# Kernel optimization log

Hardware: AMD Instinct MI355X
Metric: run time of the kernel (lower is better)

## Reference

```python
import jax, jax.numpy as jnp
import numpy as np
from jax import lax

TEMP = 20.0    # args.temp
ATT_WT = 0.5   # args.att_wt
EPS = 1e-12


def l2norm(x, axis):
    # torch F.normalize: x / max(||x||_2, eps)
    n = jnp.sqrt(jnp.sum(x * x, axis=axis, keepdims=True))
    return x / jnp.maximum(n, EPS)


def conv4d(x, w):
    """4D conv, padding=1, stride=1.
    x: [B,Cin,H1,W1,H2,W2], w: [Cout,Cin,3,3,3,3] -> [B,Cout,H1,W1,H2,W2].
    Decomposed as 9 fixed (di,dj) shifts over (H1,W1), each a 2D conv over (H2,W2).
    """
    B, Cin, H1, W1, H2, W2 = x.shape
    Cout = w.shape[0]
    xp = jnp.pad(x, ((0, 0), (0, 0), (1, 1), (1, 1), (0, 0), (0, 0)))
    out = jnp.zeros((B * H1 * W1, Cout, H2, W2), x.dtype)
    for di in range(3):
        for dj in range(3):
            xs = xp[:, :, di:di + H1, dj:dj + W1]                      # [B,Cin,H1,W1,H2,W2]
            xr = xs.transpose(0, 2, 3, 1, 4, 5).reshape(B * H1 * W1, Cin, H2, W2)
            out = out + lax.conv_general_dilated(
                xr, w[:, :, di, dj], (1, 1), 'SAME',
                dimension_numbers=('NCHW', 'OIHW', 'NCHW'))
    return out.reshape(B, H1, W1, Cout, H2, W2).transpose(0, 3, 1, 2, 4, 5)


def nc_stack(x, ws):
    for w in ws:
        x = jax.nn.relu(conv4d(x, w))
    return x


def neigh_consensus(corr, ws):
    # symmetric mode: conv(C) + perm(conv(perm(C)))
    ct = corr.transpose(0, 1, 4, 5, 2, 3)
    return nc_stack(corr, ws) + nc_stack(ct, ws).transpose(0, 1, 4, 5, 2, 3)


def setup_inputs() -> dict:
    key = jax.random.key(0)
    ks = jax.random.split(key, 7)
    L, B, C, h, w = 9, 2, 1024, 20, 20
    ch = 256
    return {
        'fq_feats': jax.random.normal(ks[0], (L, B, C, h, w), jnp.float32),
        'fs_feats': jax.random.normal(ks[1], (L, B, C, h, w), jnp.float32),
        'f_q': jax.random.normal(ks[2], (B, ch, h, w), jnp.float32),
        'f_s': jax.random.normal(ks[3], (B, ch, h, w), jnp.float32),
        'w1': jax.random.normal(ks[4], (10, 9, 3, 3, 3, 3), jnp.float32) * 0.1,
        'w2': jax.random.normal(ks[5], (10, 10, 3, 3, 3, 3), jnp.float32) * 0.1,
        'w3': jax.random.normal(ks[6], (1, 10, 3, 3, 3, 3), jnp.float32) * 0.1,
    }


def reference(fq_feats, fs_feats, f_q, f_s, w1, w2, w3):
    L, B, C, h, w = fq_feats.shape
    ch = f_q.shape[1]
    hw = h * w
    # per-level channel-wise L2 normalization -> cosine correlation volume
    fqn = l2norm(fq_feats, axis=2)
    fsn = l2norm(fs_feats, axis=2)
    # corr4d[b,l,i,j,k,m] = <fq[:, i,j], fs[:, k,m]>  -> [B, L, h, w, h, w]
    corr4d = jnp.einsum('lbcij,lbckm->blijkm', fqn, fsn)
    # neighbourhood-consensus matching net -> [B,1,h,w,h,w]
    c4 = neigh_consensus(corr4d, (w1, w2, w3))
    attn = jax.nn.softmax(c4.reshape(B, hw, hw) * TEMP, axis=-1)  # over support positions
    v = f_s.reshape(B, ch, hw)
    att_fq = jnp.einsum('bqs,bcs->bcq', attn, v).reshape(B, ch, h, w)
    fq = l2norm(f_q, axis=1) + l2norm(att_fq, axis=1) * ATT_WT
    return (fq, att_fq)
```

## Files before the change

kernel.cpp:

```cpp
#include <hip/hip_runtime.h>
#include <math.h>
#include <stddef.h>

#define L9   9
#define NB   2
#define CF   1024
#define HW   400
#define CH   256
#define TEMPF 20.0f
#define EPSF  1e-12f

typedef _Float16 half8 __attribute__((ext_vector_type(8)));
typedef float f32x4 __attribute__((ext_vector_type(4)));
typedef unsigned short ushort_t;

#define HALO_ZERO(NT)                                                          \
    for (int h = threadIdx.x; h < 84 * 20; h += (NT)) {                        \
        int rs = h / 20, c = h - rs * 20;                                      \
        int row = rs < 22 ? rs                                                 \
                : rs < 44 ? 440 + rs                                           \
                : rs < 64 ? (rs - 43) * 22                                     \
                          : (rs - 63) * 22 + 21;                               \
        ((uint*)Ah)[row * 20 + c] = 0;                                         \
    }

__global__ __launch_bounds__(256) void prep_all(const float* __restrict__ w1,
                                                const float* __restrict__ w2,
                                                const float* __restrict__ w3,
                                                const float* __restrict__ f_s,
                                                ushort_t* __restrict__ wb0,
                                                ushort_t* __restrict__ fsh,
                                                float* __restrict__ ssbuf) {
    int gid = blockIdx.x * 256 + threadIdx.x;
    if (gid < NB * CH * 416) {
        int s = gid % 416, bc = gid / 416;
        float v = (s < HW) ? f_s[(size_t)bc * HW + s] : 0.f;
        union { _Float16 h; ushort_t u; } cv; cv.h = (_Float16)v;
        fsh[gid] = cv.u;
    }
    if (gid < 14400) ssbuf[gid] = 0.f;
    if (gid < 6 * 18432) {
        int job = gid / 18432, idx = gid - job * 18432;
        int k = idx & 31, n = (idx >> 5) & 15, dd = (idx >> 9) % 9, ch = idx / 4608;
        int dk = dd / 3, dm = dd % 3;
        float v = 0.f;
        if (job < 4) {
            if (idx < 13824) {
                int CIN = (job < 2) ? 9 : 10;
                const float* wt = (job < 2) ? w1 : w2;
                bool swap = job & 1;
                int slot = ch * 32 + k;
                if (n < 10 && slot < CIN * 9) {
                    int ci = slot / 9, pl = slot - ci * 9;
                    int di = pl / 3, dj = pl % 3;
                    int widx = swap ? ((((n * CIN + ci) * 3 + dk) * 3 + dm) * 3 + di) * 3 + dj
                                    : ((((n * CIN + ci) * 3 + di) * 3 + dj) * 3 + dk) * 3 + dm;
                    v = wt[widx];
                }
                union { _Float16 h; ushort_t u; } cv; cv.h = (_Float16)v;
                wb0[job * 13824 + idx] = cv.u;
            }
        } else {
            bool swap = (job == 5);
            int slot = ch * 32 + k;
            if (slot < 120) {
                int ci = slot / 12, r = slot - ci * 12;
                int di = r >> 2, dj4 = r & 3;
                int e = dj4 - n;
                if (n < 2 && e >= 0 && e <= 2) {
                    int widx = swap ? (((ci * 3 + dk) * 3 + dm) * 3 + di) * 3 + e
                                    : (((ci * 3 + di) * 3 + e) * 3 + dk) * 3 + dm;
                    v = w3[widx];
                }
            }
            union { _Float16 h; ushort_t u; } cv; cv.h = (_Float16)v;
            wb0[55296 + (job - 4) * 18432 + idx] = cv.u;
        }
    }
}

__global__ __launch_bounds__(256) void transpose_f16(const float* __restrict__ fq,
                                                     const float* __restrict__ fs,
                                                     ushort_t* __restrict__ At,
                                                     ushort_t* __restrict__ Bt,
                                                     float* __restrict__ ssbuf,
                                                     int lb_base) {
    __shared__ float tile[64][65];
    __shared__ float red4[4][64];
    int z = blockIdx.z;
    int tsel = z / 9, li = z - tsel * 9;
    int lb = lb_base + li;
    const float* src = (tsel ? fs : fq) + (size_t)lb * CF * HW;
    ushort_t* dst = (tsel ? Bt : At) + (size_t)li * HW * CF;
    int c0 = blockIdx.x * 64, ij0 = blockIdx.y * 64;
    int tid = threadIdx.x;
    int cl = tid >> 6;
    int col = tid & 63;
    float ssp = 0.f;
    #pragma unroll
    for (int rr = 0; rr < 16; ++rr) {
        int c_local = rr * 4 + cl;
        int ij = ij0 + col;
        float v = (ij < HW) ? src[(size_t)(c0 + c_local) * HW + ij] : 0.f;
        tile[c_local][col] = v;
        ssp = fmaf(v, v, ssp);
    }
    red4[cl][col] = ssp;
    __syncthreads();
    if (cl == 0) {
        int ij = ij0 + col;
        if (ij < HW) {
            float s4 = red4[0][col] + red4[1][col] + red4[2][col] + red4[3][col];
            atomicAdd(&ssbuf[(size_t)(tsel * 18 + lb) * HW + ij], s4);
        }
    }
    int cp = (tid & 31) * 2;
    int rowsel = tid >> 5;
    #pragma unroll
    for (int rr = 0; rr < 8; ++rr) {
        int ij_local = rr * 8 + rowsel;
        int ij = ij0 + ij_local;
        if (ij < HW) {
            union { _Float16 h; ushort_t u; } h0, h1;
            h0.h = (_Float16)tile[cp][ij_local];
            h1.h = (_Float16)tile[cp + 1][ij_local];
            ushort2 o; o.x = h0.u; o.y = h1.u;
            *(ushort2*)(dst + (size_t)ij * CF + c0 + cp) = o;
        }
    }
}

__global__ __launch_bounds__(256) void corr_gemm_mfma(const ushort_t* __restrict__ At,
                                                      const ushort_t* __restrict__ Bt,
                                                      const float* __restrict__ ssbuf,
                                                      ushort_t* __restrict__ corr,
                                                      int lb_base) {
    __shared__ ushort_t As[32][72];
    __shared__ ushort_t Bs[64][72];
    int li = blockIdx.z, lb = lb_base + li;
    int l = lb >> 1, b = lb & 1;
    int i0 = blockIdx.y * 32, j0 = blockIdx.x * 64;
    int tid = threadIdx.x, lane = tid & 63, w = tid >> 6;
    int mw = (w >> 1) * 16, nw = (w & 1) * 32;
    f32x4 acc[2] = {};
    const ushort_t* Abase = At + (size_t)li * HW * CF;
    const ushort_t* Bbase = Bt + (size_t)li * HW * CF;

    for (int kt = 0; kt < 16; ++kt) {
        int c0 = kt * 64;
        __syncthreads();
        {
            int row = tid >> 3, c8 = tid & 7;
            uint4 va = make_uint4(0, 0, 0, 0);
            if (i0 + row < HW) va = *(const uint4*)(Abase + (size_t)(i0 + row) * CF + c0 + c8 * 8);
            *(uint4*)&As[row][c8 * 8] = va;
        }
        #pragma unroll
        for (int p = 0; p < 2; ++p) {
            int idx = tid + p * 256;
            int row = idx >> 3, c8 = idx & 7;
            uint4 vb = make_uint4(0, 0, 0, 0);
            if (j0 + row < HW) vb = *(const uint4*)(Bbase + (size_t)(j0 + row) * CF + c0 + c8 * 8);
            *(uint4*)&Bs[row][c8 * 8] = vb;
        }
        __syncthreads();
        #pragma unroll
        for (int ks = 0; ks < 2; ++ks) {
            int k0 = ks * 32 + (lane >> 4) * 8;
            half8 a0 = *(const half8*)&As[mw + (lane & 15)][k0];
            half8 b0 = *(const half8*)&Bs[nw + (lane & 15)][k0];
            half8 b1 = *(const half8*)&Bs[nw + 16 + (lane & 15)][k0];
            acc[0] = __builtin_amdgcn_mfma_f32_16x16x32_f16(a0, b0, acc[0], 0, 0, 0);
            acc[1] = __builtin_amdgcn_mfma_f32_16x16x32_f16(a0, b1, acc[1], 0, 0, 0);
        }
    }
    int obase = (b * 9 + l) * HW;
    #pragma unroll
    for (int ni = 0; ni < 2; ++ni) {
        int km = j0 + nw + ni * 16 + (lane & 15);
        if (km >= HW) continue;
        float ib = 1.0f / fmaxf(sqrtf(ssbuf[(size_t)(18 + lb) * HW + km]), EPSF);
        #pragma unroll
        for (int r = 0; r < 4; ++r) {
            int ij = i0 + mw + (lane >> 4) * 4 + r;
            if (ij < HW) {
                float ia = 1.0f / fmaxf(sqrtf(ssbuf[(size_t)lb * HW + ij]), EPSF);
                union { _Float16 h; ushort_t u; } cv;
                cv.h = (_Float16)(acc[ni][r] * ia * ib);
                corr[(size_t)(obase + ij) * HW + km] = cv.u;
            }
        }
    }
}

template <int CIN, int COUT, bool DUAL, bool OUTF16>
__global__ __launch_bounds__(256) void conv4d_v8h(const ushort_t* __restrict__ inA,
                                                  const ushort_t* __restrict__ inB,
                                                  const ushort_t* __restrict__ wbA,
                                                  const ushort_t* __restrict__ wbB,
                                                  void* __restrict__ outA,
                                                  void* __restrict__ outB) {
    constexpr int S = CIN * 9;
    constexpr int NCH = (S + 31) / 32;
    __shared__ __align__(16) ushort_t Ah[484 * 40];
    const int b = blockIdx.y, ij = blockIdx.x;
    const int z = blockIdx.z;
    const ushort_t* in = (DUAL || z == 0) ? inA : inB;
    const ushort_t* wbS = (DUAL || z == 0) ? wbA : wbB;
    void* outS = (DUAL || z == 0) ? outA : outB;
    const int i = ij / 20, j = ij - (ij / 20) * 20;
    const int tid = threadIdx.x, wv = tid >> 6, lane = tid & 63;
    const int m16 = lane & 15, q4 = lane >> 4;

    HALO_ZERO(256)

    int baseh[7];
    #pragma unroll
    for (int s = 0; s < 7; ++s) {
        int t = wv + 4 * s;
        if (t < 25) {
            int km = t * 16 + m16;
            int kk = km / 20, mm = km - kk * 20;
            baseh[s] = (kk * 22 + mm) * 40 + q4 * 8;
        } else baseh[s] = 0;
    }
    f32x4 accA[7] = {};
    f32x4 accB[7] = {};

    const bool stager = tid < 200;
    const int km1 = 2 * tid;
    const int r1 = stager ? ((km1 / 20 + 1) * 22 + (km1 % 20) + 1) : 0;
    int hofs[9]; bool vld[9];
    #pragma unroll
    for (int pl = 0; pl < 9; ++pl) {
        int ii = i + pl / 3 - 1, jj = j + pl % 3 - 1;
        vld[pl] = (unsigned)ii < 20u && (unsigned)jj < 20u;
        hofs[pl] = (ii * 20 + jj) * HW + km1;
    }
    const ushort_t* in_b = in + (size_t)b * CIN * HW * HW;
    const int wbase = m16 * 32 + q4 * 8;

    uint pf[32];
    #pragma unroll
    for (int u = 0; u < 32; ++u) {
        int slot = u;
        if (slot < S) {
            int ci = slot / 9, pl = slot - ci * 9;
            pf[u] = (stager && vld[pl]) ? *(const uint*)(in_b + ci * (HW * HW) + hofs[pl]) : 0u;
        } else pf[u] = 0u;
    }
    __syncthreads();

    #pragma unroll
    for (int ch = 0; ch < NCH; ++ch) {
        if (stager) {
            #pragma unroll
            for (int g4 = 0; g4 < 8; ++g4) {
                uint lo0 = (pf[4 * g4] & 0xFFFFu) | (pf[4 * g4 + 1] << 16);
                uint lo1 = (pf[4 * g4 + 2] & 0xFFFFu) | (pf[4 * g4 + 3] << 16);
                uint hi0 = (pf[4 * g4] >> 16) | (pf[4 * g4 + 1] & 0xFFFF0000u);
                uint hi1 = (pf[4 * g4 + 2] >> 16) | (pf[4 * g4 + 3] & 0xFFFF0000u);
                uint2 wlo; wlo.x = lo0; wlo.y = lo1;
                uint2 whi; whi.x = hi0; whi.y = hi1;
                *(uint2*)&Ah[(size_t)r1 * 40 + 4 * g4] = wlo;
                *(uint2*)&Ah[(size_t)(r1 + 1) * 40 + 4 * g4] = whi;
            }
        }
        __syncthreads();
        if (ch + 1 < NCH) {
            #pragma unroll
            for (int u = 0; u < 32; ++u) {
                int slot = (ch + 1) * 32 + u;
                if (slot < S) {
                    int ci = slot / 9, pl = slot - ci * 9;
                    pf[u] = (stager && vld[pl]) ? *(const uint*)(in_b + ci * (HW * HW) + hofs[pl]) : 0u;
                } else pf[u] = 0u;
            }
        }
        #pragma unroll
        for (int dd = 0; dd < 9; ++dd) {
            half8 bfA = *(const half8*)(wbS + (ch * 9 + dd) * 512 + wbase);
            half8 bfB;
            if (DUAL) bfB = *(const half8*)(wbB + (ch * 9 + dd) * 512 + wbase);
            const int doff = ((dd / 3) * 22 + (dd % 3)) * 40;
            #pragma unroll
            for (int s = 0; s < 7; ++s) {
                if (wv + 4 * s < 25) {
                    half8 af = *(const half8*)(Ah + baseh[s] + doff);
                    accA[s] = __builtin_amdgcn_mfma_f32_16x16x32_f16(af, bfA, accA[s], 0, 0, 0);
                    if (DUAL) accB[s] = __builtin_amdgcn_mfma_f32_16x16x32_f16(af, bfB, accB[s], 0, 0, 0);
                }
            }
        }
        if (ch + 1 < NCH) __syncthreads();
    }

    const int co = m16;
    if (co < COUT) {
        #pragma unroll
        for (int s = 0; s < 7; ++s) {
            int t = wv + 4 * s;
            if (t < 25) {
                int km0 = t * 16 + q4 * 4;
                size_t o = ((size_t)(b * COUT + co) * HW + ij) * HW + km0;
                if (OUTF16) {
                    union { ushort_t us[4]; uint2 u2; } pk;
                    #pragma unroll
                    for (int r = 0; r < 4; ++r) {
                        union { _Float16 h; ushort_t u16; } cv;
                        cv.h = (_Float16)fmaxf(accA[s][r], 0.f);
                        pk.us[r] = cv.u16;
                    }
                    *(uint2*)((ushort_t*)outS + o) = pk.u2;
                    if (DUAL) {
                        #pragma unroll
                        for (int r = 0; r < 4; ++r) {
                            union { _Float16 h; ushort_t u16; } cv;
                            cv.h = (_Float16)fmaxf(accB[s][r], 0.f);
                            pk.us[r] = cv.u16;
                        }
                        *(uint2*)((ushort_t*)outB + o) = pk.u2;
                    }
                } else {
                    f32x4 ov;
                    #pragma unroll
                    for (int r = 0; r < 4; ++r) ov[r] = fmaxf(accA[s][r], 0.f);
                    *(f32x4*)((float*)outS + o) = ov;
                }
            }
        }
    }
}

template <int CIN, int COUT, bool DUAL, bool OUTF16>
__global__ __launch_bounds__(512, 2) void conv4d_v14h(const ushort_t* __restrict__ inA,
                                                      const ushort_t* __restrict__ inB,
                                                      const ushort_t* __restrict__ wbA,
                                                      const ushort_t* __restrict__ wbB,
                                                      void* __restrict__ outA,
                                                      void* __restrict__ outB) {
    constexpr int S = CIN * 9;
    constexpr int NCH = (S + 31) / 32;
    __shared__ __align__(16) ushort_t Ah[484 * 40];
    const int b = blockIdx.y, ij = blockIdx.x;
    const int z = blockIdx.z;
    const ushort_t* in = (DUAL || z == 0) ? inA : inB;
    const ushort_t* wbS = (DUAL || z == 0) ? wbA : wbB;
    void* outS = (DUAL || z == 0) ? outA : outB;
    const int i = ij / 20, j = ij - (ij / 20) * 20;
    const int tid = threadIdx.x, wv = tid >> 6, lane = tid & 63;
    const int m16 = lane & 15, q4 = lane >> 4;
    const int wt = 7 - wv;

    HALO_ZERO(512)

    int baseh[4];
    #pragma unroll
    for (int s = 0; s < 4; ++s) {
        int t = wt + 8 * s;
        if (t < 25) {
            int km = t * 16 + m16;
            int kk = km / 20, mm = km - kk * 20;
            baseh[s] = (kk * 22 + mm) * 40 + q4 * 8;
        } else baseh[s] = 0;
    }
    f32x4 accA[4] = {};
    f32x4 accB[4] = {};

    const bool stager = tid < 200;
    const int km1 = 2 * tid;
    const int r1 = stager ? ((km1 / 20 + 1) * 22 + (km1 % 20) + 1) : 0;
    int hofs[9]; bool vld[9];
    #pragma unroll
    for (int pl = 0; pl < 9; ++pl) {
        int ii = i + pl / 3 - 1, jj = j + pl % 3 - 1;
        vld[pl] = (unsigned)ii < 20u && (unsigned)jj < 20u;
        hofs[pl] = (ii * 20 + jj) * HW + km1;
    }
    const ushort_t* in_b = in + (size_t)b * CIN * HW * HW;
    const int wbase = m16 * 32 + q4 * 8;

    uint pf[32];
    #pragma unroll
    for (int u = 0; u < 32; ++u) {
        int slot = u;
        if (slot < S) {
            int ci = slot / 9, pl = slot - ci * 9;
            pf[u] = (stager && vld[pl]) ? *(const uint*)(in_b + ci * (HW * HW) + hofs[pl]) : 0u;
        } else pf[u] = 0u;
    }
    __syncthreads();

    #pragma unroll
    for (int ch = 0; ch < NCH; ++ch) {
        if (stager) {
            #pragma unroll
            for (int g4 = 0; g4 < 8; ++g4) {
                uint lo0 = (pf[4 * g4] & 0xFFFFu) | (pf[4 * g4 + 1] << 16);
                uint lo1 = (pf[4 * g4 + 2] & 0xFFFFu) | (pf[4 * g4 + 3] << 16);
                uint hi0 = (pf[4 * g4] >> 16) | (pf[4 * g4 + 1] & 0xFFFF0000u);
                uint hi1 = (pf[4 * g4 + 2] >> 16) | (pf[4 * g4 + 3] & 0xFFFF0000u);
                uint2 wlo; wlo.x = lo0; wlo.y = lo1;
                uint2 whi; whi.x = hi0; whi.y = hi1;
                *(uint2*)&Ah[(size_t)r1 * 40 + 4 * g4] = wlo;
                *(uint2*)&Ah[(size_t)(r1 + 1) * 40 + 4 * g4] = whi;
            }
        }
        __syncthreads();
        if (ch + 1 < NCH) {
            #pragma unroll
            for (int u = 0; u < 32; ++u) {
                int slot = (ch + 1) * 32 + u;
                if (slot < S) {
                    int ci = slot / 9, pl = slot - ci * 9;
                    pf[u] = (stager && vld[pl]) ? *(const uint*)(in_b + ci * (HW * HW) + hofs[pl]) : 0u;
                } else pf[u] = 0u;
            }
        }
        #pragma unroll
        for (int dd = 0; dd < 9; ++dd) {
            half8 bfA = *(const half8*)(wbS + (ch * 9 + dd) * 512 + wbase);
            half8 bfB;
            if (DUAL) bfB = *(const half8*)(wbB + (ch * 9 + dd) * 512 + wbase);
            const int doff = ((dd / 3) * 22 + (dd % 3)) * 40;
            #pragma unroll
            for (int s = 0; s < 4; ++s) {
                if (wt + 8 * s < 25) {
                    half8 af = *(const half8*)(Ah + baseh[s] + doff);
                    accA[s] = __builtin_amdgcn_mfma_f32_16x16x32_f16(af, bfA, accA[s], 0, 0, 0);
                    if (DUAL) accB[s] = __builtin_amdgcn_mfma_f32_16x16x32_f16(af, bfB, accB[s], 0, 0, 0);
                }
            }
        }
        if (ch + 1 < NCH) __syncthreads();
    }

    const int co = m16;
    if (co < COUT) {
        #pragma unroll
        for (int s = 0; s < 4; ++s) {
            int t = wt + 8 * s;
            if (t < 25) {
                int km0 = t * 16 + q4 * 4;
                size_t o = ((size_t)(b * COUT + co) * HW + ij) * HW + km0;
                if (OUTF16) {
                    union { ushort_t us[4]; uint2 u2; } pk;
                    #pragma unroll
                    for (int r = 0; r < 4; ++r) {
                        union { _Float16 h; ushort_t u16; } cv;
                        cv.h = (_Float16)fmaxf(accA[s][r], 0.f);
                        pk.us[r] = cv.u16;
                    }
                    *(uint2*)((ushort_t*)outS + o) = pk.u2;
                    if (DUAL) {
                        #pragma unroll
                        for (int r = 0; r < 4; ++r) {
                            union { _Float16 h; ushort_t u16; } cv;
                            cv.h = (_Float16)fmaxf(accB[s][r], 0.f);
                            pk.us[r] = cv.u16;
                        }
                        *(uint2*)((ushort_t*)outB + o) = pk.u2;
                    }
                } else {
                    f32x4 ov;
                    #pragma unroll
                    for (int r = 0; r < 4; ++r) ov[r] = fmaxf(accA[s][r], 0.f);
                    *(f32x4*)((float*)outS + o) = ov;
                }
            }
        }
    }
}

template <int CIN>
__global__ __launch_bounds__(512, 2) void conv4d_l3(
        const ushort_t* __restrict__ inA, const ushort_t* __restrict__ inB,
        const ushort_t* __restrict__ wAm, const ushort_t* __restrict__ wBm,
        float* __restrict__ outA, float* __restrict__ outB) {
    constexpr int S2 = CIN * 12;
    constexpr int NCH = (S2 + 31) / 32;
    __shared__ __align__(16) ushort_t Ah[484 * 40];
    const int b = blockIdx.y, bx = blockIdx.x, z = blockIdx.z;
    const ushort_t* in = z ? inB : inA;
    const ushort_t* w1 = z ? wBm : wAm;
    float* outS = z ? outB : outA;
    const int i = bx / 10, jp = bx - (bx / 10) * 10;
    const int j0 = 2 * jp;
    const int ij0 = i * 20 + j0;
    const int tid = threadIdx.x, wv = tid >> 6, lane = tid & 63;
    const int m16 = lane & 15, q4 = lane >> 4;
    const int wt = 7 - wv;

    HALO_ZERO(512)

    int baseh[4];
    #pragma unroll
    for (int s = 0; s < 4; ++s) {
        int t = wt + 8 * s;
        if (t < 25) {
            int km = t * 16 + m16;
            int kk = km / 20, mm = km - kk * 20;
            baseh[s] = (kk * 22 + mm) * 40 + q4 * 8;
        } else baseh[s] = 0;
    }
    f32x4 acc1[4] = {};

    const bool stager = tid < 200;
    const int km1 = 2 * tid;
    const int r1 = stager ? ((km1 / 20 + 1) * 22 + (km1 % 20) + 1) : 0;
    int hofs[12]; bool vld[12];
    #pragma unroll
    for (int pl = 0; pl < 12; ++pl) {
        int di = pl >> 2, dj = pl & 3;
        int ii = i + di - 1, jj = j0 + dj - 1;
        vld[pl] = (unsigned)ii < 20u && (unsigned)jj < 20u;
        hofs[pl] = (ii * 20 + jj) * HW + km1;
    }
    const ushort_t* in_b = in + (size_t)b * CIN * HW * HW;
    const int wbase = m16 * 32 + q4 * 8;

    uint pf[32];
    #pragma unroll
    for (int u = 0; u < 32; ++u) {
        int slot = u;
        if (slot < S2) {
            int ci = slot / 12, pl = slot - ci * 12;
            pf[u] = (stager && vld[pl]) ? *(const uint*)(in_b + ci * (HW * HW) + hofs[pl]) : 0u;
        } else pf[u] = 0u;
    }
    __syncthreads();

    #pragma unroll
    for (int ch = 0; ch < NCH; ++ch) {
        if (stager) {
            #pragma unroll
            for (int g4 = 0; g4 < 8; ++g4) {
                uint lo0 = (pf[4 * g4] & 0xFFFFu) | (pf[4 * g4 + 1] << 16);
                uint lo1 = (pf[4 * g4 + 2] & 0xFFFFu) | (pf[4 * g4 + 3] << 16);
                uint hi0 = (pf[4 * g4] >> 16) | (pf[4 * g4 + 1] & 0xFFFF0000u);
                uint hi1 = (pf[4 * g4 + 2] >> 16) | (pf[4 * g4 + 3] & 0xFFFF0000u);
                uint2 wlo; wlo.x = lo0; wlo.y = lo1;
                uint2 whi; whi.x = hi0; whi.y = hi1;
                *(uint2*)&Ah[(size_t)r1 * 40 + 4 * g4] = wlo;
                *(uint2*)&Ah[(size_t)(r1 + 1) * 40 + 4 * g4] = whi;
            }
        }
        __syncthreads();
        if (ch + 1 < NCH) {
            #pragma unroll
            for (int u = 0; u < 32; ++u) {
                int slot = (ch + 1) * 32 + u;
                if (slot < S2) {
                    int ci = slot / 12, pl = slot - ci * 12;
                    pf[u] = (stager && vld[pl]) ? *(const uint*)(in_b + ci * (HW * HW) + hofs[pl]) : 0u;
                } else pf[u] = 0u;
            }
        }
        #pragma unroll
        for (int dd = 0; dd < 9; ++dd) {
            half8 bf1 = *(const half8*)(w1 + (ch * 9 + dd) * 512 + wbase);
            const int doff = ((dd / 3) * 22 + (dd % 3)) * 40;
            #pragma unroll
            for (int s = 0; s < 4; ++s) {
                if (wt + 8 * s < 25) {
                    half8 af = *(const half8*)(Ah + baseh[s] + doff);
                    acc1[s] = __builtin_amdgcn_mfma_f32_16x16x32_f16(af, bf1, acc1[s], 0, 0, 0);
                }
            }
        }
        if (ch + 1 < NCH) __syncthreads();
    }

    if (m16 < 2) {
        const int ij = ij0 + m16;
        #pragma unroll
        for (int s = 0; s < 4; ++s) {
            int t = wt + 8 * s;
            if (t < 25) {
                int km0 = t * 16 + q4 * 4;
                size_t o = ((size_t)b * HW + ij) * HW + km0;
                f32x4 ov;
                #pragma unroll
                for (int r = 0; r < 4; ++r) ov[r] = fmaxf(acc1[s][r], 0.f);
                *(f32x4*)(outS + o) = ov;
            }
        }
    }
}

__global__ __launch_bounds__(256) void softmax_av_mfma3(const float* __restrict__ c4A,
                                                        const float* __restrict__ c4B,
                                                        const ushort_t* __restrict__ fsh,
                                                        float* __restrict__ att) {
    __shared__ ushort_t P[32 * 424];
    __shared__ float invl[32];
    const int b = blockIdx.z, qb = blockIdx.x * 32;
    const int tid = threadIdx.x, wv = tid >> 6, lane = tid & 63;
    const int m16 = lane & 15, q4 = lane >> 4;
    const int lane16 = lane & 15, rg4 = lane >> 4;

    #pragma unroll 1
    for (int rg = 0; rg < 2; ++rg) {
        const int ql = wv * 8 + rg * 4 + rg4;
        int q = qb + ql; if (q > HW - 1) q = HW - 1;
        const float* rowA = c4A + ((size_t)b * HW + q) * HW;
        const float* rowB = c4B + ((size_t)b * HW + q) * HW;
        float4 v4[7];
        #pragma unroll
        for (int k4 = 0; k4 < 6; ++k4) {
            float4 a4 = *(const float4*)(rowA + 64 * k4 + lane16 * 4);
            float4 b4 = *(const float4*)(rowB + 64 * k4 + lane16 * 4);
            v4[k4] = make_float4(a4.x + b4.x, a4.y + b4.y, a4.z + b4.z, a4.w + b4.w);
        }
        if (lane16 < 4) {
            float4 a4 = *(const float4*)(rowA + 384 + lane16 * 4);
            float4 b4 = *(const float4*)(rowB + 384 + lane16 * 4);
            v4[6] = make_float4(a4.x + b4.x, a4.y + b4.y, a4.z + b4.z, a4.w + b4.w);
        } else {
            v4[6] = make_float4(-1e30f, -1e30f, -1e30f, -1e30f);
        }
        float mx = -1e30f;
        #pragma unroll
        for (int k4 = 0; k4 < 7; ++k4)
            mx = fmaxf(mx, fmaxf(fmaxf(v4[k4].x, v4[k4].y), fmaxf(v4[k4].z, v4[k4].w)));
        #pragma unroll
        for (int off = 8; off; off >>= 1) mx = fmaxf(mx, __shfl_xor(mx, off, 16));
        float sum = 0.f;
        #pragma unroll
        for (int k4 = 0; k4 < 7; ++k4) {
            if (k4 == 6 && lane16 >= 4) break;
            float e0 = __expf(TEMPF * (v4[k4].x - mx));
            float e1 = __expf(TEMPF * (v4[k4].y - mx));
            float e2 = __expf(TEMPF * (v4[k4].z - mx));
            float e3 = __expf(TEMPF * (v4[k4].w - mx));
            sum += e0 + e1 + e2 + e3;
            union { ushort_t us[4]; uint2 u2; } pk;
            union { _Float16 h; ushort_t u16; } cv;
            cv.h = (_Float16)e0; pk.us[0] = cv.u16;
            cv.h = (_Float16)e1; pk.us[1] = cv.u16;
            cv.h = (_Float16)e2; pk.us[2] = cv.u16;
            cv.h = (_Float16)e3; pk.us[3] = cv.u16;
            *(uint2*)&P[(size_t)ql * 424 + 64 * k4 + lane16 * 4] = pk.u2;
        }
        if (lane16 >= 4 && lane16 < 10) {
            uint2 z2; z2.x = 0; z2.y = 0;
            *(uint2*)&P[(size_t)ql * 424 + 384 + lane16 * 4] = z2;
        }
        #pragma unroll
        for (int off = 8; off; off >>= 1) sum += __shfl_xor(sum, off, 16);
        if (lane16 == 0) invl[ql] = 1.0f / sum;
    }
    __syncthreads();

    const int mtile = wv & 1, ntl = wv >> 1;
    half8 afr[13];
    #pragma unroll
    for (int ks = 0; ks < 13; ++ks)
        afr[ks] = *(const half8*)&P[(size_t)(mtile * 16 + m16) * 424 + ks * 32 + q4 * 8];
    const ushort_t* fb = fsh + (size_t)b * CH * 416;
    const int nt = blockIdx.y * 2 + ntl;
    const int c = nt * 16 + m16;
    const ushort_t* fc = fb + (size_t)c * 416 + q4 * 8;
    f32x4 acc = {};
    #pragma unroll
    for (int ks = 0; ks < 13; ++ks) {
        half8 bf = *(const half8*)(fc + ks * 32);
        acc = __builtin_amdgcn_mfma_f32_16x16x32_f16(afr[ks], bf, acc, 0, 0, 0);
    }
    #pragma unroll
    for (int r = 0; r < 4; ++r) {
        int ql = mtile * 16 + q4 * 4 + r;
        int q = qb + ql;
        if (q < HW)
            att[((size_t)b * CH + c) * HW + q] = acc[r] * invl[ql];
    }
}

__global__ __launch_bounds__(256) void final_fq(const float* __restrict__ f_q,
                                                const float* __restrict__ att,
                                                float* __restrict__ out_fq) {
    __shared__ float2 red[4];
    int b = blockIdx.y, q = blockIdx.x;
    int tid = threadIdx.x, wv = tid >> 6, lane = tid & 63;
    size_t idx = (size_t)(b * CH + tid) * HW + q;
    float f = f_q[idx];
    float a = att[idx];
    float vf = f * f, va = a * a;
    #pragma unroll
    for (int off = 32; off; off >>= 1) {
        vf += __shfl_xor(vf, off);
        va += __shfl_xor(va, off);
    }
    if (lane == 0) red[wv] = make_float2(vf, va);
    __syncthreads();
    float sf = red[0].x + red[1].x + red[2].x + red[3].x;
    float sa = red[0].y + red[1].y + red[2].y + red[3].y;
    float invf = 1.0f / fmaxf(sqrtf(sf), EPSF);
    float inva = 1.0f / fmaxf(sqrtf(sa), EPSF);
    out_fq[idx] = f * invf + 0.5f * a * inva;
}

extern "C" void kernel_launch(void* const* d_in, const int* in_sizes, int n_in,
                              void* d_out, int out_size, void* d_ws, size_t ws_size,
                              hipStream_t stream) {
    const float* fq_feats = (const float*)d_in[0];
    const float* fs_feats = (const float*)d_in[1];
    const float* f_q      = (const float*)d_in[2];
    const float* f_s      = (const float*)d_in[3];
    const float* w1       = (const float*)d_in[4];
    const float* w2       = (const float*)d_in[5];
    const float* w3       = (const float*)d_in[6];
    float* out = (float*)d_out;

    float* ws      = (float*)d_ws;
    float* wbuf    = ws;
    float* ssbuf   = wbuf + 115200;
    float* corr    = ssbuf + 14400;
    float* buf1    = corr + 2880000;
    float* buf2    = buf1 + 3200000;
    float* att     = out + 204800;

    ushort_t* corr_h = (ushort_t*)corr;
    ushort_t* fsh    = (ushort_t*)(corr + 1440000);
    float* c4A = corr + 1600000;
    float* c4B = corr + 1920000;
    ushort_t* At = (ushort_t*)buf1;
    ushort_t* Bt = (ushort_t*)buf2;
    ushort_t* b1A = (ushort_t*)buf1;
    ushort_t* b1B = b1A + 3200000;
    ushort_t* b2A = (ushort_t*)buf2;
    ushort_t* b2B = b2A + 3200000;

    ushort_t* wb0   = (ushort_t*)wbuf;
    ushort_t* wbL1A = wb0;
    ushort_t* wbL1B = wb0 + 13824;
    ushort_t* wbL2A = wb0 + 27648;
    ushort_t* wbL2B = wb0 + 41472;
    ushort_t* wbL3Am = wb0 + 55296;
    ushort_t* wbL3Bm = wb0 + 73728;

    prep_all<<<832, 256, 0, stream>>>(w1, w2, w3, f_s, wb0, fsh, ssbuf);

    for (int half = 0; half < 2; ++half) {
        int base = half * 9;
        transpose_f16<<<dim3(16, 7, 18), 256, 0, stream>>>(fq_feats, fs_feats, At, Bt, ssbuf, base);
        corr_gemm_mfma<<<dim3(7, 13, 9), 256, 0, stream>>>(At, Bt, ssbuf, corr_h, base);
    }

    conv4d_v14h<9, 10, true, true><<<dim3(400, NB, 1), 512, 0, stream>>>(
        corr_h, corr_h, wbL1A, wbL1B, b1A, b1B);
    conv4d_v8h<10, 10, false, true><<<dim3(400, NB, 2), 256, 0, stream>>>(
        b1A, b1B, wbL2A, wbL2B, b2A, b2B);
    conv4d_l3<10><<<dim3(200, NB, 2), 512, 0, stream>>>(
        b2A, b2B, wbL3Am, wbL3Bm, c4A, c4B);

    softmax_av_mfma3<<<dim3(13, 8, NB), 256, 0, stream>>>(c4A, c4B, fsh, att);
    final_fq<<<dim3(400, NB), 256, 0, stream>>>(f_q, att, out);

    (void)in_sizes; (void)n_in; (void)out_size; (void)ws_size;
}
```

Measured before the change: 331.2 us.

## Fuse final 4D conv layer with softmax and attention-value GEMM

Merges the third conv4d layer (both symmetric branches) with the softmax and the attention×V product into one kernel. Each block computes two query rows for both branches, sums them in shared memory, applies the softmax, and runs MFMA against the fp16 support features to write att directly. This removes the c4A/c4B fp32 round trip and one kernel launch. The cost is that the grid halves (z dimension dropped), each block runs the two branch convolutions back to back, and each block rereads the full fsh matrix for only two queries, with 14 of 16 MFMA rows wasted.

After: 329.1 us. About the same (-0.6%).

```diff
diff --git a/kernel.cpp b/kernel.cpp
--- a/kernel.cpp
+++ b/kernel.cpp
@@ -473,17 +473,17 @@
 }
 
 template <int CIN>
-__global__ __launch_bounds__(512, 2) void conv4d_l3(
-        const ushort_t* __restrict__ inA, const ushort_t* __restrict__ inB,
+__global__ __launch_bounds__(512, 2) void conv4d_l3f(
+        const ushort_t* __restrict__ b2A, const ushort_t* __restrict__ b2B,
         const ushort_t* __restrict__ wAm, const ushort_t* __restrict__ wBm,
-        float* __restrict__ outA, float* __restrict__ outB) {
+        const ushort_t* __restrict__ fsh, float* __restrict__ att) {
     constexpr int S2 = CIN * 12;
     constexpr int NCH = (S2 + 31) / 32;
     __shared__ __align__(16) ushort_t Ah[484 * 40];
-    const int b = blockIdx.y, bx = blockIdx.x, z = blockIdx.z;
-    const ushort_t* in = z ? inB : inA;
-    const ushort_t* w1 = z ? wBm : wAm;
-    float* outS = z ? outB : outA;
+    __shared__ float rows[2][400];
+    __shared__ __align__(16) ushort_t P[16][416];
+    __shared__ float invl[2];
+    const int b = blockIdx.y, bx = blockIdx.x;
     const int i = bx / 10, jp = bx - (bx / 10) * 10;
     const int j0 = 2 * jp;
     const int ij0 = i * 20 + j0;
@@ -503,7 +503,7 @@
             baseh[s] = (kk * 22 + mm) * 40 + q4 * 8;
         } else baseh[s] = 0;
     }
-    f32x4 acc1[4] = {};
+    f32x4 acc[2][4] = {};
 
     const bool stager = tid < 200;
     const int km1 = 2 * tid;
@@ -516,163 +516,130 @@
         vld[pl] = (unsigned)ii < 20u && (unsigned)jj < 20u;
         hofs[pl] = (ii * 20 + jj) * HW + km1;
     }
-    const ushort_t* in_b = in + (size_t)b * CIN * HW * HW;
     const int wbase = m16 * 32 + q4 * 8;
-
     uint pf[32];
-    #pragma unroll
-    for (int u = 0; u < 32; ++u) {
-        int slot = u;
-        if (slot < S2) {
-            int ci = slot / 12, pl = slot - ci * 12;
-            pf[u] = (stager && vld[pl]) ? *(const uint*)(in_b + ci * (HW * HW) + hofs[pl]) : 0u;
-        } else pf[u] = 0u;
-    }
-    __syncthreads();
-
-    #pragma unroll
-    for (int ch = 0; ch < NCH; ++ch) {
-        if (stager) {
+
+    #pragma unroll
+    for (int p = 0; p < 2; ++p) {
+        const ushort_t* in_b = (p ? b2B : b2A) + (size_t)b * CIN * HW * HW;
+        const ushort_t* wm = p ? wBm : wAm;
+        #pragma unroll
+        for (int u = 0; u < 32; ++u) {
+            int slot = u;
+            if (slot < S2) {
+                int ci = slot / 12, pl = slot - ci * 12;
+                pf[u] = (stager && vld[pl]) ? *(const uint*)(in_b + ci * (HW * HW) + hofs[pl]) : 0u;
+            } else pf[u] = 0u;
+        }
+        __syncthreads();
+
+        #pragma unroll
+        for (int ch = 0; ch < NCH; ++ch) {
+            if (stager) {
+                #pragma unroll
+                for (int g4 = 0; g4 < 8; ++g4) {
+                    uint lo0 = (pf[4 * g4] & 0xFFFFu) | (pf[4 * g4 + 1] << 16);
+                    uint lo1 = (pf[4 * g4 + 2] & 0xFFFFu) | (pf[4 * g4 + 3] << 16);
+                    uint hi0 = (pf[4 * g4] >> 16) | (pf[4 * g4 + 1] & 0xFFFF0000u);
+                    uint hi1 = (pf[4 * g4 + 2] >> 16) | (pf[4 * g4 + 3] & 0xFFFF0000u);
+                    uint2 wlo; wlo.x = lo0; wlo.y = lo1;
+                    uint2 whi; whi.x = hi0; whi.y = hi1;
+                    *(uint2*)&Ah[(size_t)r1 * 40 + 4 * g4] = wlo;
+                    *(uint2*)&Ah[(size_t)(r1 + 1) * 40 + 4 * g4] = whi;
+                }
+            }
+            __syncthreads();
+            if (ch + 1 < NCH) {
+                #pragma unroll
+                for (int u = 0; u < 32; ++u) {
+                    int slot = (ch + 1) * 32 + u;
+                    if (slot < S2) {
+                        int ci = slot / 12, pl = slot - ci * 12;
+                        pf[u] = (stager && vld[pl]) ? *(const uint*)(in_b + ci * (HW * HW) + hofs[pl]) : 0u;
+                    } else pf[u] = 0u;
+                }
+            }
             #pragma unroll
-            for (int g4 = 0; g4 < 8; ++g4) {
-                uint lo0 = (pf[4 * g4] & 0xFFFFu) | (pf[4 * g4 + 1] << 16);
-                uint lo1 = (pf[4 * g4 + 2] & 0xFFFFu) | (pf[4 * g4 + 3] << 16);
-                uint hi0 = (pf[4 * g4] >> 16) | (pf[4 * g4 + 1] & 0xFFFF0000u);
-                uint hi1 = (pf[4 * g4 + 2] >> 16) | (pf[4 * g4 + 3] & 0xFFFF0000u);
-                uint2 wlo; wlo.x = lo0; wlo.y = lo1;
-                uint2 whi; whi.x = hi0; whi.y = hi1;
-                *(uint2*)&Ah[(size_t)r1 * 40 + 4 * g4] = wlo;
-                *(uint2*)&Ah[(size_t)(r1 + 1) * 40 + 4 * g4] = whi;
-            }
-        }
-        __syncthreads();
-        if (ch + 1 < NCH) {
-            #pragma unroll
-            for (int u = 0; u < 32; ++u) {
-                int slot = (ch + 1) * 32 + u;
-                if (slot < S2) {
-                    int ci = slot / 12, pl = slot - ci * 12;
-                    pf[u] = (stager && vld[pl]) ? *(const uint*)(in_b + ci * (HW * HW) + hofs[pl]) : 0u;
-                } else pf[u] = 0u;
-            }
-        }
-        #pragma unroll
-        for (int dd = 0; dd < 9; ++dd) {
-            half8 bf1 = *(const half8*)(w1 + (ch * 9 + dd) * 512 + wbase);
-            const int doff = ((dd / 3) * 22 + (dd % 3)) * 40;
-            #pragma unroll
-            for (int s = 0; s < 4; ++s) {
-                if (wt + 8 * s < 25) {
-                    half8 af = *(const half8*)(Ah + baseh[s] + doff);
-                    acc1[s] = __builtin_amdgcn_mfma_f32_16x16x32_f16(af, bf1, acc1[s], 0, 0, 0);
-                }
-            }
-        }
-        if (ch + 1 < NCH) __syncthreads();
+            for (int dd = 0; dd < 9; ++dd) {
+                half8 bf1 = *(const half8*)(wm + (ch * 9 + dd) * 512 + wbase);
+                const int doff = ((dd / 3) * 22 + (dd % 3)) * 40;
+                #pragma unroll
+                for (int s = 0; s < 4; ++s) {
+                    if (wt + 8 * s < 25) {
+                        half8 af = *(const half8*)(Ah + baseh[s] + doff);
+                        acc[p][s] = __builtin_amdgcn_mfma_f32_16x16x32_f16(af, bf1, acc[p][s], 0, 0, 0);
+                    }
+                }
+            }
+            if (ch + 1 < NCH) __syncthreads();
+        }
     }
 
     if (m16 < 2) {
-        const int ij = ij0 + m16;
         #pragma unroll
         for (int s = 0; s < 4; ++s) {
             int t = wt + 8 * s;
             if (t < 25) {
                 int km0 = t * 16 + q4 * 4;
-                size_t o = ((size_t)b * HW + ij) * HW + km0;
-                f32x4 ov;
                 #pragma unroll
-                for (int r = 0; r < 4; ++r) ov[r] = fmaxf(acc1[s][r], 0.f);
-                *(f32x4*)(outS + o) = ov;
-            }
-        }
-    }
-}
-
-__global__ __launch_bounds__(256) void softmax_av_mfma3(const float* __restrict__ c4A,
-                                                        const float* __restrict__ c4B,
-                                                        const ushort_t* __restrict__ fsh,
-                                                        float* __restrict__ att) {
-    __shared__ ushort_t P[32 * 424];
-    __shared__ float invl[32];
-    const int b = blockIdx.z, qb = blockIdx.x * 32;
-    const int tid = threadIdx.x, wv = tid >> 6, lane = tid & 63;
-    const int m16 = lane & 15, q4 = lane >> 4;
-    const int lane16 = lane & 15, rg4 = lane >> 4;
-
-    #pragma unroll 1
-    for (int rg = 0; rg < 2; ++rg) {
-        const int ql = wv * 8 + rg * 4 + rg4;
-        int q = qb + ql; if (q > HW - 1) q = HW - 1;
-        const float* rowA = c4A + ((size_t)b * HW + q) * HW;
-        const float* rowB = c4B + ((size_t)b * HW + q) * HW;
-        float4 v4[7];
-        #pragma unroll
-        for (int k4 = 0; k4 < 6; ++k4) {
-            float4 a4 = *(const float4*)(rowA + 64 * k4 + lane16 * 4);
-            float4 b4 = *(const float4*)(rowB + 64 * k4 + lane16 * 4);
-            v4[k4] = make_float4(a4.x + b4.x, a4.y + b4.y, a4.z + b4.z, a4.w + b4.w);
-        }
-        if (lane16 < 4) {
-            float4 a4 = *(const float4*)(rowA + 384 + lane16 * 4);
-            float4 b4 = *(const float4*)(rowB + 384 + lane16 * 4);
-            v4[6] = make_float4(a4.x + b4.x, a4.y + b4.y, a4.z + b4.z, a4.w + b4.w);
-        } else {
-            v4[6] = make_float4(-1e30f, -1e30f, -1e30f, -1e30f);
-        }
+                for (int r = 0; r < 4; ++r)
+                    rows[m16][km0 + r] = fmaxf(acc[0][s][r], 0.f) + fmaxf(acc[1][s][r], 0.f);
+            }
+        }
+    }
+    __syncthreads();
+
+    if (wv < 2) {
+        const int q = wv;
+        float v[7];
         float mx = -1e30f;
         #pragma unroll
-        for (int k4 = 0; k4 < 7; ++k4)
-            mx = fmaxf(mx, fmaxf(fmaxf(v4[k4].x, v4[k4].y), fmaxf(v4[k4].z, v4[k4].w)));
-        #pragma unroll
-        for (int off = 8; off; off >>= 1) mx = fmaxf(mx, __shfl_xor(mx, off, 16));
+        for (int u = 0; u < 7; ++u) {
+            int k = lane + 64 * u;
+            v[u] = (k < HW) ? rows[q][k] : -1e30f;
+            mx = fmaxf(mx, v[u]);
+        }
+        #pragma unroll
+        for (int off = 32; off; off >>= 1) mx = fmaxf(mx, __shfl_xor(mx, off));
         float sum = 0.f;
         #pragma unroll
-        for (int k4 = 0; k4 < 7; ++k4) {
-            if (k4 == 6 && lane16 >= 4) break;
-            float e0 = __expf(TEMPF * (v4[k4].x - mx));
-            float e1 = __expf(TEMPF * (v4[k4].y - mx));
-            float e2 = __expf(TEMPF * (v4[k4].z - mx));
-            float e3 = __expf(TEMPF * (v4[k4].w - mx));
-            sum += e0 + e1 + e2 + e3;
-            union { ushort_t us[4]; uint2 u2; } pk;
-            union { _Float16 h; ushort_t u16; } cv;
-            cv.h = (_Float16)e0; pk.us[0] = cv.u16;
-            cv.h = (_Float16)e1; pk.us[1] = cv.u16;
-            cv.h = (_Float16)e2; pk.us[2] = cv.u16;
-            cv.h = (_Float16)e3; pk.us[3] = cv.u16;
-            *(uint2*)&P[(size_t)ql * 424 + 64 * k4 + lane16 * 4] = pk.u2;
-        }
-        if (lane16 >= 4 && lane16 < 10) {
-            uint2 z2; z2.x = 0; z2.y = 0;
-            *(uint2*)&P[(size_t)ql * 424 + 384 + lane16 * 4] = z2;
-        }
-        #pragma unroll
-        for (int off = 8; off; off >>= 1) sum += __shfl_xor(sum, off, 16);
-        if (lane16 == 0) invl[ql] = 1.0f / sum;
+        for (int u = 0; u < 7; ++u) {
+            int k = lane + 64 * u;
+            if (k < HW) {
+                float e = __expf(TEMPF * (v[u] - mx));
+                sum += e;
+                union { _Float16 h; ushort_t u16; } cv; cv.h = (_Float16)e;
+                P[q][k] = cv.u16;
+            }
+        }
+        if (lane < 16) P[q][400 + lane] = 0;
+        #pragma unroll
+        for (int off = 32; off; off >>= 1) sum += __shfl_xor(sum, off);
+        if (lane == 0) invl[q] = 1.0f / sum;
     }
     __syncthreads();
 
-    const int mtile = wv & 1, ntl = wv >> 1;
-    half8 afr[13];
-    #pragma unroll
-    for (int ks = 0; ks < 13; ++ks)
-        afr[ks] = *(const half8*)&P[(size_t)(mtile * 16 + m16) * 424 + ks * 32 + q4 * 8];
     const ushort_t* fb = fsh + (size_t)b * CH * 416;
-    const int nt = blockIdx.y * 2 + ntl;
-    const int c = nt * 16 + m16;
-    const ushort_t* fc = fb + (size_t)c * 416 + q4 * 8;
-    f32x4 acc = {};
-    #pragma unroll
-    for (int ks = 0; ks < 13; ++ks) {
-        half8 bf = *(const half8*)(fc + ks * 32);
-        acc = __builtin_amdgcn_mfma_f32_16x16x32_f16(afr[ks], bf, acc, 0, 0, 0);
-    }
-    #pragma unroll
-    for (int r = 0; r < 4; ++r) {
-        int ql = mtile * 16 + q4 * 4 + r;
-        int q = qb + ql;
-        if (q < HW)
-            att[((size_t)b * CH + c) * HW + q] = acc[r] * invl[ql];
+    #pragma unroll
+    for (int tt = 0; tt < 2; ++tt) {
+        const int ct = wv * 2 + tt;
+        const ushort_t* fc = fb + (size_t)(ct * 16 + m16) * 416 + q4 * 8;
+        f32x4 acc2 = {};
+        #pragma unroll
+        for (int ks = 0; ks < 13; ++ks) {
+            half8 afr = *(const half8*)(fc + ks * 32);
+            half8 bfr = *(const half8*)&P[m16][ks * 32 + q4 * 8];
+            acc2 = __builtin_amdgcn_mfma_f32_16x16x32_f16(afr, bfr, acc2, 0, 0, 0);
+        }
+        if (m16 < 2) {
+            const int q = ij0 + m16;
+            const float il = invl[m16];
+            #pragma unroll
+            for (int r = 0; r < 4; ++r) {
+                int c = ct * 16 + q4 * 4 + r;
+                att[((size_t)(b * CH + c)) * HW + q] = acc2[r] * il;
+            }
+        }
     }
 }
 
@@ -722,8 +689,6 @@
 
     ushort_t* corr_h = (ushort_t*)corr;
     ushort_t* fsh    = (ushort_t*)(corr + 1440000);
-    float* c4A = corr + 1600000;
-    float* c4B = corr + 1920000;
     ushort_t* At = (ushort_t*)buf1;
     ushort_t* Bt = (ushort_t*)buf2;
     ushort_t* b1A = (ushort_t*)buf1;
@@ -751,10 +716,9 @@
         corr_h, corr_h, wbL1A, wbL1B, b1A, b1B);
     conv4d_v8h<10, 10, false, true><<<dim3(400, NB, 2), 256, 0, stream>>>(
         b1A, b1B, wbL2A, wbL2B, b2A, b2B);
-    conv4d_l3<10><<<dim3(200, NB, 2), 512, 0, stream>>>(
-        b2A, b2B, wbL3Am, wbL3Bm, c4A, c4B);
-
-    softmax_av_mfma3<<<dim3(13, 8, NB), 256, 0, stream>>>(c4A, c4B, fsh, att);
+    conv4d_l3f<10><<<dim3(200, NB), 512, 0, stream>>>(
+        b2A, b2B, wbL3Am, wbL3Bm, fsh, att);
+
     final_fq<<<dim3(400, NB), 256, 0, stream>>>(f_q, att, out);
 
     (void)in_sizes; (void)n_in; (void)out_size; (void)ws_size;
```
